# Optimization experiments

Measured on AMD Instinct MI355X. Metric: run time of the kernel, lower is better.

## Reference

```python
import jax, jax.numpy as jnp
import numpy as np

SCALE = 5.656854249492381  # sqrt(head_dim=32)


def setup_inputs() -> dict:
    key = jax.random.key(0)
    kq, kk, kv = jax.random.split(key, 3)
    shape = (16, 16, 256, 32)  # [batch, heads, seq, head_dim]
    q = jax.random.normal(kq, shape, dtype=jnp.float16)
    k = jax.random.normal(kk, shape, dtype=jnp.float16)
    v = jax.random.normal(kv, shape, dtype=jnp.float16)
    return {"q": q, "k": k, "v": v}


def reference(q, k, v):
    # scores = q @ k^T / sqrt(d): [b, h, s, s], fp16 matmul then fp32 softmax
    scores = jnp.einsum("bhqd,bhkd->bhqk", q, k) / jnp.float16(SCALE)
    probs = jax.nn.softmax(scores.astype(jnp.float32), axis=-1).astype(jnp.float16)
    out = jnp.einsum("bhqk,bhkd->bhqd", probs, v)  # [b, h, s, d]
    return (out,)
```

## Files before the change

### kernel.cpp

```cpp
#include <hip/hip_runtime.h>


typedef _Float16 f16;
typedef f16 f16x4 __attribute__((ext_vector_type(4)));
typedef f16 f16x8 __attribute__((ext_vector_type(8)));
typedef float f32x4 __attribute__((ext_vector_type(4)));
typedef f16x8 f16x8_u __attribute__((may_alias));
typedef f16x4 f16x4_u __attribute__((may_alias));
typedef f32x4 f32x4_u __attribute__((may_alias));

#define SEQ 256
#define HD 32
#define KP 40
#define SP 264

__global__ __launch_bounds__(256, 2)
void attn_kernel(const float* __restrict__ Q, const float* __restrict__ K,
                 const float* __restrict__ V, float* __restrict__ O)
{
    __shared__ __align__(16) f16 Ks[SEQ][KP];
    __shared__ __align__(16) f16 Vt[HD][SP];
    __shared__ __align__(16) f16 Pb[4][16][SP];

    const int tid  = threadIdx.x;
    const int wave = tid >> 6;
    const int lane = tid & 63;
    const int l15  = lane & 15;
    const int quad = lane >> 4;

    const int slice = blockIdx.x & 255;
    const int half  = blockIdx.x >> 8;

    const size_t base = (size_t)slice * (SEQ * HD);
    const float* q = Q + base;
    const float* k = K + base;
    const float* v = V + base;
    float*       o = O + base;

    #pragma unroll
    for (int it = 0; it < 8; ++it) {
        int vec = tid + it * 256;
        int r = vec >> 3;
        int c = (vec & 7) << 2;
        f32x4 kv = *(const f32x4_u*)(k + r * HD + c);
        f32x4 vv = *(const f32x4_u*)(v + r * HD + c);
        f16x4 kh;
        #pragma unroll
        for (int j = 0; j < 4; ++j) kh[j] = (f16)kv[j];
        *(f16x4_u*)(&Ks[r][c]) = kh;
        #pragma unroll
        for (int j = 0; j < 4; ++j) Vt[c + j][r] = (f16)vv[j];
    }
    __syncthreads();

    f16x8 vb[8][2];
    #pragma unroll
    for (int c = 0; c < 8; ++c)
        #pragma unroll
        for (int h = 0; h < 2; ++h)
            vb[c][h] = *(const f16x8_u*)(&Vt[h * 16 + l15][c * 32 + quad * 8]);

    const float C_EXP = 1.44269504088896f / 5.65625f;

    #pragma unroll 1
    for (int qi = 0; qi < 2; ++qi) {
        const int qt = half * 8 + wave * 2 + qi;
        const float* qp = q + (qt * 16 + l15) * HD + quad * 8;
        f32x4 a = *(const f32x4_u*)(qp);
        f32x4 b = *(const f32x4_u*)(qp + 4);
        f16x8 qa;
        #pragma unroll
        for (int j = 0; j < 4; ++j) { qa[j] = (f16)a[j]; qa[4 + j] = (f16)b[j]; }

        float sum = 0.f;
        #pragma unroll
        for (int kt = 0; kt < 16; ++kt) {
            f16x8 kf = *(const f16x8_u*)(&Ks[kt * 16 + l15][quad * 8]);
            f32x4 z = {0.f, 0.f, 0.f, 0.f};
            f32x4 s = __builtin_amdgcn_mfma_f32_16x16x32_f16(kf, qa, z, 0, 0, 0);
            f16x4 ph;
            #pragma unroll
            for (int r = 0; r < 4; ++r) {
                float e = __builtin_amdgcn_exp2f(s[r] * C_EXP);
                sum += e;
                ph[r] = (f16)e;
            }
            *(f16x4_u*)(&Pb[wave][l15][kt * 16 + quad * 4]) = ph;
        }
        sum += __shfl_xor(sum, 16);
        sum += __shfl_xor(sum, 32);
        const float rs = 1.0f / sum;

        f32x4 o0 = {0.f, 0.f, 0.f, 0.f};
        f32x4 o1 = {0.f, 0.f, 0.f, 0.f};
        #pragma unroll
        for (int c = 0; c < 8; ++c) {
            f16x8 pa = *(const f16x8_u*)(&Pb[wave][l15][c * 32 + quad * 8]);
            o0 = __builtin_amdgcn_mfma_f32_16x16x32_f16(pa, vb[c][0], o0, 0, 0, 0);
            o1 = __builtin_amdgcn_mfma_f32_16x16x32_f16(pa, vb[c][1], o1, 0, 0, 0);
        }

        #pragma unroll
        for (int r4 = 0; r4 < 4; ++r4) {
            const float rsr = __shfl(rs, quad * 4 + r4);
            const int row = qt * 16 + quad * 4 + r4;
            o[row * HD + l15]      = (float)(f16)(o0[r4] * rsr);
            o[row * HD + 16 + l15] = (float)(f16)(o1[r4] * rsr);
        }
    }
}

extern "C" void kernel_launch(void* const* d_in, const int* in_sizes, int n_in,
                              void* d_out, int out_size, void* d_ws, size_t ws_size,
                              hipStream_t stream) {
    const float* q = (const float*)d_in[0];
    const float* k = (const float*)d_in[1];
    const float* v = (const float*)d_in[2];
    float* o = (float*)d_out;
    const int bh = in_sizes[0] / (SEQ * HD);
    attn_kernel<<<bh * 2, 256, 0, stream>>>(q, k, v, o);
}
```

Measured before the change: 78.60 us.

## Keep softmax probabilities in registers via permlane swaps and split slices across 4 blocks

Drops the per-wave shared-memory P buffer. The exponentiated scores are packed to fp16 and redistributed across lanes with v_permlane32/16_swap so they can feed the PV MFMA directly as the A operand. Each block now handles a quarter of a slice with one query tile per wave, and the grid doubles. Launch bounds are raised to 4 blocks per CU, and V fragments are reloaded from LDS inside the PV loop instead of being held in registers. In exchange, the K/V staging from global memory is repeated twice as often per slice.

```diff
diff --git a/kernel.cpp b/kernel.cpp
--- a/kernel.cpp
+++ b/kernel.cpp
@@ -2,6 +2,7 @@
 
 
 typedef _Float16 f16;
+typedef f16 f16x2 __attribute__((ext_vector_type(2)));
 typedef f16 f16x4 __attribute__((ext_vector_type(4)));
 typedef f16 f16x8 __attribute__((ext_vector_type(8)));
 typedef float f32x4 __attribute__((ext_vector_type(4)));
@@ -14,13 +15,17 @@
 #define KP 40
 #define SP 264
 
-__global__ __launch_bounds__(256, 2)
+static __device__ __forceinline__ unsigned pack2(float a, float b) {
+    f16x2 h; h[0] = (f16)a; h[1] = (f16)b;
+    return __builtin_bit_cast(unsigned, h);
+}
+
+__global__ __launch_bounds__(256, 4)
 void attn_kernel(const float* __restrict__ Q, const float* __restrict__ K,
                  const float* __restrict__ V, float* __restrict__ O)
 {
     __shared__ __align__(16) f16 Ks[SEQ][KP];
     __shared__ __align__(16) f16 Vt[HD][SP];
-    __shared__ __align__(16) f16 Pb[4][16][SP];
 
     const int tid  = threadIdx.x;
     const int wave = tid >> 6;
@@ -29,7 +34,7 @@
     const int quad = lane >> 4;
 
     const int slice = blockIdx.x & 255;
-    const int half  = blockIdx.x >> 8;
+    const int part  = blockIdx.x >> 8;
 
     const size_t base = (size_t)slice * (SEQ * HD);
     const float* q = Q + base;
@@ -53,60 +58,70 @@
     }
     __syncthreads();
 
-    f16x8 vb[8][2];
-    #pragma unroll
-    for (int c = 0; c < 8; ++c)
-        #pragma unroll
-        for (int h = 0; h < 2; ++h)
-            vb[c][h] = *(const f16x8_u*)(&Vt[h * 16 + l15][c * 32 + quad * 8]);
-
     const float C_EXP = 1.44269504088896f / 5.65625f;
 
-    #pragma unroll 1
-    for (int qi = 0; qi < 2; ++qi) {
-        const int qt = half * 8 + wave * 2 + qi;
-        const float* qp = q + (qt * 16 + l15) * HD + quad * 8;
-        f32x4 a = *(const f32x4_u*)(qp);
-        f32x4 b = *(const f32x4_u*)(qp + 4);
-        f16x8 qa;
+    const int qt = part * 4 + wave;
+
+    const float* qp = q + (qt * 16 + l15) * HD + quad * 8;
+    f32x4 a = *(const f32x4_u*)(qp);
+    f32x4 b = *(const f32x4_u*)(qp + 4);
+    f16x8 qa;
+    #pragma unroll
+    for (int j = 0; j < 4; ++j) { qa[j] = (f16)a[j]; qa[4 + j] = (f16)b[j]; }
+
+    float sum = 0.f;
+    unsigned pw[8][4];
+    #pragma unroll
+    for (int c = 0; c < 8; ++c) {
+        f16x8 kf0 = *(const f16x8_u*)(&Ks[(c * 2 + 0) * 16 + l15][quad * 8]);
+        f16x8 kf1 = *(const f16x8_u*)(&Ks[(c * 2 + 1) * 16 + l15][quad * 8]);
+        f32x4 z = {0.f, 0.f, 0.f, 0.f};
+        f32x4 s0 = __builtin_amdgcn_mfma_f32_16x16x32_f16(kf0, qa, z, 0, 0, 0);
+        f32x4 s1 = __builtin_amdgcn_mfma_f32_16x16x32_f16(kf1, qa, z, 0, 0, 0);
+        float e[8];
         #pragma unroll
-        for (int j = 0; j < 4; ++j) { qa[j] = (f16)a[j]; qa[4 + j] = (f16)b[j]; }
+        for (int r = 0; r < 4; ++r) e[r]     = __builtin_amdgcn_exp2f(s0[r] * C_EXP);
+        #pragma unroll
+        for (int r = 0; r < 4; ++r) e[4 + r] = __builtin_amdgcn_exp2f(s1[r] * C_EXP);
+        #pragma unroll
+        for (int r = 0; r < 8; ++r) sum += e[r];
+        unsigned d0 = pack2(e[0], e[1]);
+        unsigned d1 = pack2(e[2], e[3]);
+        unsigned d2 = pack2(e[4], e[5]);
+        unsigned d3 = pack2(e[6], e[7]);
+        asm("v_permlane32_swap_b32 %0, %1" : "+v"(d0), "+v"(d2));
+        asm("v_permlane32_swap_b32 %0, %1" : "+v"(d1), "+v"(d3));
+        asm("v_permlane16_swap_b32 %0, %1" : "+v"(d0), "+v"(d2));
+        asm("v_permlane16_swap_b32 %0, %1" : "+v"(d1), "+v"(d3));
+        pw[c][0] = d0;
+        pw[c][1] = d1;
+        pw[c][2] = d2;
+        pw[c][3] = d3;
+    }
+    sum += __shfl_xor(sum, 16);
+    sum += __shfl_xor(sum, 32);
+    const float rs = 1.0f / sum;
 
-        float sum = 0.f;
-        #pragma unroll
-        for (int kt = 0; kt < 16; ++kt) {
-            f16x8 kf = *(const f16x8_u*)(&Ks[kt * 16 + l15][quad * 8]);
-            f32x4 z = {0.f, 0.f, 0.f, 0.f};
-            f32x4 s = __builtin_amdgcn_mfma_f32_16x16x32_f16(kf, qa, z, 0, 0, 0);
-            f16x4 ph;
-            #pragma unroll
-            for (int r = 0; r < 4; ++r) {
-                float e = __builtin_amdgcn_exp2f(s[r] * C_EXP);
-                sum += e;
-                ph[r] = (f16)e;
-            }
-            *(f16x4_u*)(&Pb[wave][l15][kt * 16 + quad * 4]) = ph;
-        }
-        sum += __shfl_xor(sum, 16);
-        sum += __shfl_xor(sum, 32);
-        const float rs = 1.0f / sum;
+    f32x4 o0 = {0.f, 0.f, 0.f, 0.f};
+    f32x4 o1 = {0.f, 0.f, 0.f, 0.f};
+    #pragma unroll
+    for (int c = 0; c < 8; ++c) {
+        union { unsigned u[4]; f16x8 v; } pu;
+        pu.u[0] = pw[c][0]; pu.u[1] = pw[c][1];
+        pu.u[2] = pw[c][2]; pu.u[3] = pw[c][3];
+        f16x8 pa  = pu.v;
+        f16x8 vb0 = *(const f16x8_u*)(&Vt[l15][c * 32 + quad * 8]);
+        f16x8 vb1 = *(const f16x8_u*)(&Vt[16 + l15][c * 32 + quad * 8]);
+        o0 = __builtin_amdgcn_mfma_f32_16x16x32_f16(pa, vb0, o0, 0, 0, 0);
+        o1 = __builtin_amdgcn_mfma_f32_16x16x32_f16(pa, vb1, o1, 0, 0, 0);
+    }
 
-        f32x4 o0 = {0.f, 0.f, 0.f, 0.f};
-        f32x4 o1 = {0.f, 0.f, 0.f, 0.f};
-        #pragma unroll
-        for (int c = 0; c < 8; ++c) {
-            f16x8 pa = *(const f16x8_u*)(&Pb[wave][l15][c * 32 + quad * 8]);
-            o0 = __builtin_amdgcn_mfma_f32_16x16x32_f16(pa, vb[c][0], o0, 0, 0, 0);
-            o1 = __builtin_amdgcn_mfma_f32_16x16x32_f16(pa, vb[c][1], o1, 0, 0, 0);
-        }
-
-        #pragma unroll
-        for (int r4 = 0; r4 < 4; ++r4) {
-            const float rsr = __shfl(rs, quad * 4 + r4);
-            const int row = qt * 16 + quad * 4 + r4;
-            o[row * HD + l15]      = (float)(f16)(o0[r4] * rsr);
-            o[row * HD + 16 + l15] = (float)(f16)(o1[r4] * rsr);
-        }
+    #pragma unroll
+    for (int r4 = 0; r4 < 4; ++r4) {
+        const float rsr = __shfl(rs, quad * 4 + r4);
+        const int row = qt * 16 + quad * 4 + r4;
+        o[row * HD + l15]      = (float)(f16)(o0[r4] * rsr);
+        o[row * HD + 16 + l15] = (float)(f16)(o1[r4] * rsr);
     }
 }
 
@@ -118,5 +133,5 @@
     const float* v = (const float*)d_in[2];
     float* o = (float*)d_out;
     const int bh = in_sizes[0] / (SEQ * HD);
-    attn_kernel<<<bh * 2, 256, 0, stream>>>(q, k, v, o);
+    attn_kernel<<<bh * 4, 256, 0, stream>>>(q, k, v, o);
 }
```

Result: no change. 79.12 us (+0.7%).
